# Optimization experiments

Measured on AMD Instinct MI355X. Metric: run time of the kernel, lower is better.

The kernel has to match this reference:

```python
import jax, jax.numpy as jnp
import numpy as np

B, L, C = 32, 4096, 64
PL, PC = 64, 16          # patch sizes along L and C
NP = 256                 # num_patches
OUT = 512                # output_dim
FS = 1000.0              # sampling frequency -> T = 1/FS


def setup_inputs() -> dict:
    key = jax.random.key(0)
    ks = jax.random.split(key, 7)
    d_in = PL * (PC * 2)
    return {
        "x": jax.random.normal(ks[0], (B, L, C), dtype=jnp.float32),
        "start_L": jax.random.randint(ks[1], (B, NP), 0, L - PL + 1, dtype=jnp.int32),
        "start_C": jax.random.randint(ks[2], (B, NP), 0, C - PC + 1, dtype=jnp.int32),
        "w1": jax.random.normal(ks[3], (OUT, d_in), dtype=jnp.float32) / np.sqrt(d_in),
        "b1": jax.random.normal(ks[4], (OUT,), dtype=jnp.float32) * 0.01,
        "w2": jax.random.normal(ks[5], (OUT, OUT), dtype=jnp.float32) / np.sqrt(OUT),
        "b2": jax.random.normal(ks[6], (OUT,), dtype=jnp.float32) * 0.01,
    }


def reference(x, start_L, start_C, w1, b1, w2, b2):
    T = 1.0 / FS
    t = jnp.arange(L, dtype=jnp.float32) * T                      # [L]

    # patch index grids (wrapping, as in the torch module)
    idx_L = (start_L[:, :, None] + jnp.arange(PL, dtype=jnp.int32)) % L   # [B,NP,PL]
    idx_C = (start_C[:, :, None] + jnp.arange(PC, dtype=jnp.int32)) % C   # [B,NP,PC]

    # double gather: patches[b,p,i,j] = x[b, idx_L[b,p,i], idx_C[b,p,j]]
    b_idx = jnp.arange(B, dtype=jnp.int32)[:, None, None, None]
    patches = x[b_idx, idx_L[:, :, :, None], idx_C[:, :, None, :]]        # [B,NP,PL,PC]

    # time embedding gathered with the same L indices, broadcast over PC
    t_patches = jnp.broadcast_to(t[idx_L][:, :, :, None], (B, NP, PL, PC))

    feats = jnp.concatenate([patches, t_patches], axis=-1)                # [B,NP,PL,2*PC]
    feats = feats.reshape(B, NP, PL * 2 * PC)

    h = jnp.einsum('bpd,od->bpo', feats, w1) + b1
    h = jax.nn.silu(h)
    out = jnp.einsum('bpo,qo->bpq', h, w2) + b2                           # [B,NP,OUT]
    return out
```

## Files before the change

kernel.cpp:

```cpp
#include <hip/hip_runtime.h>
#include <hip/hip_bf16.h>
#include <stdint.h>

#define BB   32
#define LL   4096
#define CCH  64
#define PLh  64
#define PCh  16
#define NPp  256
#define DOUT 512
#define DINX 1024
#define MM   (BB * NPp)
#define TT   0.001f

using bf16 = __hip_bfloat16;
typedef __attribute__((ext_vector_type(8))) short bf16x8;
typedef __attribute__((ext_vector_type(4))) float f32x4;

__device__ __forceinline__ void async_copy16(void* lds, const void* g) {
    __builtin_amdgcn_global_load_lds(
        (const __attribute__((address_space(1))) void*)g,
        (__attribute__((address_space(3))) void*)lds,
        16, 0, 0);
}

__global__ __launch_bounds__(256) void convert_f32_bf16(
    const float* __restrict__ in, bf16* __restrict__ out, int n)
{
    int i = (blockIdx.x * 256 + threadIdx.x) * 4;
    if (i >= n) return;
    float4 v = *(const float4*)(in + i);
    union { bf16 h[4]; uint2 u; } p;
    p.h[0] = __float2bfloat16(v.x);
    p.h[1] = __float2bfloat16(v.y);
    p.h[2] = __float2bfloat16(v.z);
    p.h[3] = __float2bfloat16(v.w);
    *(uint2*)(out + i) = p.u;
}

__global__ __launch_bounds__(256) void convert_w1x(
    const float* __restrict__ w1, bf16* __restrict__ w1x)
{
    int i = (blockIdx.x * 256 + threadIdx.x) * 4;
    int o = i >> 10, r = i & 1023;
    int l = r >> 4, j = r & 15;
    float4 v = *(const float4*)(w1 + (size_t)o * 2048 + l * 32 + j);
    union { bf16 h[4]; uint2 u; } p;
    p.h[0] = __float2bfloat16(v.x);
    p.h[1] = __float2bfloat16(v.y);
    p.h[2] = __float2bfloat16(v.z);
    p.h[3] = __float2bfloat16(v.w);
    *(uint2*)(w1x + i) = p.u;
}

__global__ __launch_bounds__(64) void precompute_affine(
    const float* __restrict__ w1, const float* __restrict__ b1,
    float* __restrict__ A1, float* __restrict__ C1)
{
    const int o = blockIdx.x;
    const int l = threadIdx.x;
    const float* wr = w1 + (size_t)o * 2048 + l * 32 + 16;
    float s0 = 0.f;
#pragma unroll
    for (int j = 0; j < 16; ++j) s0 += wr[j];
    float s1 = (float)l * s0;
#pragma unroll
    for (int off = 32; off > 0; off >>= 1) {
        s0 += __shfl_down(s0, off);
        s1 += __shfl_down(s1, off);
    }
    if (l == 0) {
        A1[o] = TT * s0;
        C1[o] = b1[o] + TT * s1;
    }
}

__global__ __launch_bounds__(256) void gather_feats(
    const float* __restrict__ x, const int* __restrict__ startL,
    const int* __restrict__ startC, bf16* __restrict__ feats)
{
    const int m = blockIdx.x;
    const int b = m >> 8;
    const int t = threadIdx.x;
    const int l = t >> 2;
    const int j0 = (t & 3) * 4;
    const int sl = startL[m];
    const int sc = startC[m];
    const float* src = x + ((size_t)b * LL + (size_t)(sl + l)) * CCH + sc + j0;
    union { bf16 h[4]; uint2 u; } p;
#pragma unroll
    for (int i = 0; i < 4; ++i) p.h[i] = __float2bfloat16(src[i]);
    *(uint2*)(feats + (size_t)m * DINX + t * 4) = p.u;
}

template <bool FUSE1>
__global__ __launch_bounds__(256) void gemm_bt(
    const bf16* __restrict__ A,
    const bf16* __restrict__ Bt,
    const float* __restrict__ bias,
    const float* __restrict__ C1,
    const int*   __restrict__ sL,
    void* __restrict__ outp,
    const int N, const int K)
{
    constexpr int BK = 32;
    __shared__ __align__(16) bf16 As[64 * BK];
    __shared__ __align__(16) bf16 Bs[64 * BK];

    const int tid  = threadIdx.x;
    const int lane = tid & 63;
    const int wave = tid >> 6;
    const int row0 = blockIdx.x * 64;
    const int col0 = blockIdx.y * 64;

    const int  srow  = wave * 16 + (lane >> 2);
    const int  skoff = (lane & 3) * 8;
    const bf16* agp = A  + (size_t)(row0 + srow) * K + skoff;
    const bf16* bgp = Bt + (size_t)(col0 + srow) * K + skoff;
    bf16* as_dst = &As[wave * 16 * BK];
    bf16* bs_dst = &Bs[wave * 16 * BK];

    const int mw = (wave >> 1) * 32;
    const int nw = (wave & 1) * 32;
    const int fr = lane & 15;
    const int fq = lane >> 4;

    f32x4 acc[2][2] = {};

    for (int k0 = 0; k0 < K; k0 += BK) {
        __syncthreads();
        async_copy16(as_dst, agp + k0);
        async_copy16(bs_dst, bgp + k0);
        __syncthreads();

        bf16x8 af[2], bfm[2];
#pragma unroll
        for (int i = 0; i < 2; ++i)
            af[i] = *(const bf16x8*)&As[(mw + i * 16 + fr) * BK + fq * 8];
#pragma unroll
        for (int j = 0; j < 2; ++j)
            bfm[j] = *(const bf16x8*)&Bs[(nw + j * 16 + fr) * BK + fq * 8];
#pragma unroll
        for (int i = 0; i < 2; ++i)
#pragma unroll
            for (int j = 0; j < 2; ++j)
                acc[i][j] = __builtin_amdgcn_mfma_f32_16x16x32_bf16(
                    af[i], bfm[j], acc[i][j], 0, 0, 0);
    }

    float slr[2][4];
    if (FUSE1) {
#pragma unroll
        for (int i = 0; i < 2; ++i)
#pragma unroll
            for (int r = 0; r < 4; ++r)
                slr[i][r] = (float)sL[row0 + mw + i * 16 + fq * 4 + r];
    }

#pragma unroll
    for (int j = 0; j < 2; ++j) {
        const int col = col0 + nw + j * 16 + fr;
        const float bv = bias[col];
        const float cv = FUSE1 ? C1[col] : 0.f;
#pragma unroll
        for (int i = 0; i < 2; ++i) {
#pragma unroll
            for (int r = 0; r < 4; ++r) {
                const int row = row0 + mw + i * 16 + fq * 4 + r;
                float v;
                if (FUSE1) {
                    v = acc[i][j][r] + slr[i][r] * bv + cv;
                    v = v / (1.0f + __expf(-v));
                    ((bf16*)outp)[(size_t)row * N + col] = __float2bfloat16(v);
                } else {
                    v = acc[i][j][r] + bv;
                    ((float*)outp)[(size_t)row * N + col] = v;
                }
            }
        }
    }
}

extern "C" void kernel_launch(void* const* d_in, const int* in_sizes, int n_in,
                              void* d_out, int out_size, void* d_ws, size_t ws_size,
                              hipStream_t stream)
{
    const float* x  = (const float*)d_in[0];
    const int*   sL = (const int*)  d_in[1];
    const int*   sC = (const int*)  d_in[2];
    const float* w1 = (const float*)d_in[3];
    const float* b1 = (const float*)d_in[4];
    const float* w2 = (const float*)d_in[5];
    const float* b2 = (const float*)d_in[6];
    float* out = (float*)d_out;

    char* ws = (char*)d_ws;
    bf16* featsB = (bf16*)ws;
    size_t off = (size_t)MM * DINX * 2;
    bf16* w1xB = (bf16*)(ws + off); off += (size_t)DOUT * DINX * 2;
    bf16* w2B  = (bf16*)(ws + off); off += (size_t)DOUT * DOUT * 2;
    bf16* hB   = (bf16*)(ws + off); off += (size_t)MM * DOUT * 2;
    float* A1  = (float*)(ws + off); off += DOUT * 4;
    float* C1  = (float*)(ws + off);

    convert_w1x<<<(DOUT * DINX / 4 + 255) / 256, 256, 0, stream>>>(w1, w1xB);
    convert_f32_bf16<<<(DOUT * DOUT / 4 + 255) / 256, 256, 0, stream>>>(w2, w2B, DOUT * DOUT);
    precompute_affine<<<DOUT, 64, 0, stream>>>(w1, b1, A1, C1);
    gather_feats<<<MM, 256, 0, stream>>>(x, sL, sC, featsB);

    gemm_bt<true><<<dim3(MM / 64, DOUT / 64), 256, 0, stream>>>(
        featsB, w1xB, A1, C1, sL, hB, DOUT, DINX);

    gemm_bt<false><<<dim3(MM / 64, DOUT / 64), 256, 0, stream>>>(
        hB, w2B, b2, nullptr, nullptr, out, DOUT, DOUT);
}
```

Before: 133.7 us.

## Double-buffer GEMM with BK=64, merge prep kernels, vectorize gather

The GEMM kernel now uses BK=64 with two LDS buffers, issuing the async global-to-LDS loads for the next K tile while the current tile's MFMAs run, and drops one barrier per iteration. The three weight-preparation kernels are merged into a single launch. The gather kernel now has one thread per patch row doing four float4 loads and two 16-byte stores. These changes aim to cut the load-latency stalls, barrier count and launch overhead in exchange for more LDS per block; relying on the single barrier to order async LDS writes against reads of the other buffer is a potential hazard.

```diff
diff --git a/kernel.cpp b/kernel.cpp
--- a/kernel.cpp
+++ b/kernel.cpp
@@ -5,8 +5,6 @@
 #define BB   32
 #define LL   4096
 #define CCH  64
-#define PLh  64
-#define PCh  16
 #define NPp  256
 #define DOUT 512
 #define DINX 1024
@@ -24,54 +22,49 @@
         16, 0, 0);
 }
 
-__global__ __launch_bounds__(256) void convert_f32_bf16(
-    const float* __restrict__ in, bf16* __restrict__ out, int n)
-{
-    int i = (blockIdx.x * 256 + threadIdx.x) * 4;
-    if (i >= n) return;
-    float4 v = *(const float4*)(in + i);
+__device__ __forceinline__ uint2 pack4_bf16(float a, float b, float c, float d) {
     union { bf16 h[4]; uint2 u; } p;
-    p.h[0] = __float2bfloat16(v.x);
-    p.h[1] = __float2bfloat16(v.y);
-    p.h[2] = __float2bfloat16(v.z);
-    p.h[3] = __float2bfloat16(v.w);
-    *(uint2*)(out + i) = p.u;
-}
-
-__global__ __launch_bounds__(256) void convert_w1x(
-    const float* __restrict__ w1, bf16* __restrict__ w1x)
-{
-    int i = (blockIdx.x * 256 + threadIdx.x) * 4;
-    int o = i >> 10, r = i & 1023;
-    int l = r >> 4, j = r & 15;
-    float4 v = *(const float4*)(w1 + (size_t)o * 2048 + l * 32 + j);
-    union { bf16 h[4]; uint2 u; } p;
-    p.h[0] = __float2bfloat16(v.x);
-    p.h[1] = __float2bfloat16(v.y);
-    p.h[2] = __float2bfloat16(v.z);
-    p.h[3] = __float2bfloat16(v.w);
-    *(uint2*)(w1x + i) = p.u;
-}
-
-__global__ __launch_bounds__(64) void precompute_affine(
+    p.h[0] = __float2bfloat16(a);
+    p.h[1] = __float2bfloat16(b);
+    p.h[2] = __float2bfloat16(c);
+    p.h[3] = __float2bfloat16(d);
+    return p.u;
+}
+
+__global__ __launch_bounds__(256) void prep(
     const float* __restrict__ w1, const float* __restrict__ b1,
+    const float* __restrict__ w2,
+    bf16* __restrict__ w1x, bf16* __restrict__ w2b,
     float* __restrict__ A1, float* __restrict__ C1)
 {
-    const int o = blockIdx.x;
-    const int l = threadIdx.x;
-    const float* wr = w1 + (size_t)o * 2048 + l * 32 + 16;
-    float s0 = 0.f;
-#pragma unroll
-    for (int j = 0; j < 16; ++j) s0 += wr[j];
-    float s1 = (float)l * s0;
-#pragma unroll
-    for (int off = 32; off > 0; off >>= 1) {
-        s0 += __shfl_down(s0, off);
-        s1 += __shfl_down(s1, off);
-    }
-    if (l == 0) {
-        A1[o] = TT * s0;
-        C1[o] = b1[o] + TT * s1;
+    const int blk = blockIdx.x;
+    if (blk < 512) {
+        int i = (blk * 256 + threadIdx.x) * 4;
+        int o = i >> 10, r = i & 1023;
+        int l = r >> 4, j = r & 15;
+        float4 v = *(const float4*)(w1 + (size_t)o * 2048 + l * 32 + j);
+        *(uint2*)(w1x + i) = pack4_bf16(v.x, v.y, v.z, v.w);
+    } else if (blk < 768) {
+        int i = ((blk - 512) * 256 + threadIdx.x) * 4;
+        float4 v = *(const float4*)(w2 + i);
+        *(uint2*)(w2b + i) = pack4_bf16(v.x, v.y, v.z, v.w);
+    } else {
+        const int o = (blk - 768) * 4 + (threadIdx.x >> 6);
+        const int l = threadIdx.x & 63;
+        const float* wr = w1 + (size_t)o * 2048 + l * 32 + 16;
+        float s0 = 0.f;
+#pragma unroll
+        for (int j = 0; j < 16; ++j) s0 += wr[j];
+        float s1 = (float)l * s0;
+#pragma unroll
+        for (int off = 32; off > 0; off >>= 1) {
+            s0 += __shfl_down(s0, off);
+            s1 += __shfl_down(s1, off);
+        }
+        if (l == 0) {
+            A1[o] = TT * s0;
+            C1[o] = b1[o] + TT * s1;
+        }
     }
 }
 
@@ -79,33 +72,41 @@
     const float* __restrict__ x, const int* __restrict__ startL,
     const int* __restrict__ startC, bf16* __restrict__ feats)
 {
-    const int m = blockIdx.x;
+    const int m = blockIdx.x * 4 + (threadIdx.x >> 6);
     const int b = m >> 8;
-    const int t = threadIdx.x;
-    const int l = t >> 2;
-    const int j0 = (t & 3) * 4;
+    const int l = threadIdx.x & 63;
     const int sl = startL[m];
     const int sc = startC[m];
-    const float* src = x + ((size_t)b * LL + (size_t)(sl + l)) * CCH + sc + j0;
-    union { bf16 h[4]; uint2 u; } p;
-#pragma unroll
-    for (int i = 0; i < 4; ++i) p.h[i] = __float2bfloat16(src[i]);
-    *(uint2*)(feats + (size_t)m * DINX + t * 4) = p.u;
+    const float* src = x + ((size_t)b * LL + (size_t)(sl + l)) * CCH + sc;
+    float4 v0 = *(const float4*)(src);
+    float4 v1 = *(const float4*)(src + 4);
+    float4 v2 = *(const float4*)(src + 8);
+    float4 v3 = *(const float4*)(src + 12);
+    uint4 p0, p1;
+    uint2 a = pack4_bf16(v0.x, v0.y, v0.z, v0.w);
+    uint2 c = pack4_bf16(v1.x, v1.y, v1.z, v1.w);
+    p0.x = a.x; p0.y = a.y; p0.z = c.x; p0.w = c.y;
+    a = pack4_bf16(v2.x, v2.y, v2.z, v2.w);
+    c = pack4_bf16(v3.x, v3.y, v3.z, v3.w);
+    p1.x = a.x; p1.y = a.y; p1.z = c.x; p1.w = c.y;
+    bf16* dst = feats + (size_t)m * DINX + l * 16;
+    *(uint4*)dst       = p0;
+    *(uint4*)(dst + 8) = p1;
 }
 
 template <bool FUSE1>
-__global__ __launch_bounds__(256) void gemm_bt(
+__global__ __launch_bounds__(256, 4) void gemm_db(
     const bf16* __restrict__ A,
     const bf16* __restrict__ Bt,
-    const float* __restrict__ bias,
+    const float* __restrict__ P1,
     const float* __restrict__ C1,
     const int*   __restrict__ sL,
     void* __restrict__ outp,
     const int N, const int K)
 {
-    constexpr int BK = 32;
-    __shared__ __align__(16) bf16 As[64 * BK];
-    __shared__ __align__(16) bf16 Bs[64 * BK];
+    constexpr int BK = 64;
+    __shared__ __align__(16) bf16 As[2][64 * BK];
+    __shared__ __align__(16) bf16 Bs[2][64 * BK];
 
     const int tid  = threadIdx.x;
     const int lane = tid & 63;
@@ -113,12 +114,11 @@
     const int row0 = blockIdx.x * 64;
     const int col0 = blockIdx.y * 64;
 
-    const int  srow  = wave * 16 + (lane >> 2);
-    const int  skoff = (lane & 3) * 8;
+    const int  srow  = wave * 16 + (lane >> 3);
+    const int  skoff = (lane & 7) * 8;
     const bf16* agp = A  + (size_t)(row0 + srow) * K + skoff;
     const bf16* bgp = Bt + (size_t)(col0 + srow) * K + skoff;
-    bf16* as_dst = &As[wave * 16 * BK];
-    bf16* bs_dst = &Bs[wave * 16 * BK];
+    const int w16 = wave * 16;
 
     const int mw = (wave >> 1) * 32;
     const int nw = (wave & 1) * 32;
@@ -127,25 +127,44 @@
 
     f32x4 acc[2][2] = {};
 
-    for (int k0 = 0; k0 < K; k0 += BK) {
+    const int nIter = K / BK;
+
+    async_copy16(&As[0][(w16 + 0) * BK], agp);
+    async_copy16(&As[0][(w16 + 8) * BK], agp + (size_t)8 * K);
+    async_copy16(&Bs[0][(w16 + 0) * BK], bgp);
+    async_copy16(&Bs[0][(w16 + 8) * BK], bgp + (size_t)8 * K);
+
+    for (int it = 0; it < nIter; ++it) {
         __syncthreads();
-        async_copy16(as_dst, agp + k0);
-        async_copy16(bs_dst, bgp + k0);
-        __syncthreads();
-
-        bf16x8 af[2], bfm[2];
+        const int cur = it & 1;
+        if (it + 1 < nIter) {
+            const int nxt = cur ^ 1;
+            const int k1 = (it + 1) * BK;
+            async_copy16(&As[nxt][(w16 + 0) * BK], agp + k1);
+            async_copy16(&As[nxt][(w16 + 8) * BK], agp + (size_t)8 * K + k1);
+            async_copy16(&Bs[nxt][(w16 + 0) * BK], bgp + k1);
+            async_copy16(&Bs[nxt][(w16 + 8) * BK], bgp + (size_t)8 * K + k1);
+        }
+
+        bf16x8 af[2][2], bfr[2][2];
 #pragma unroll
         for (int i = 0; i < 2; ++i)
-            af[i] = *(const bf16x8*)&As[(mw + i * 16 + fr) * BK + fq * 8];
+#pragma unroll
+            for (int ks = 0; ks < 2; ++ks)
+                af[i][ks] = *(const bf16x8*)&As[cur][(mw + i * 16 + fr) * BK + ks * 32 + fq * 8];
 #pragma unroll
         for (int j = 0; j < 2; ++j)
-            bfm[j] = *(const bf16x8*)&Bs[(nw + j * 16 + fr) * BK + fq * 8];
-#pragma unroll
-        for (int i = 0; i < 2; ++i)
-#pragma unroll
-            for (int j = 0; j < 2; ++j)
-                acc[i][j] = __builtin_amdgcn_mfma_f32_16x16x32_bf16(
-                    af[i], bfm[j], acc[i][j], 0, 0, 0);
+#pragma unroll
+            for (int ks = 0; ks < 2; ++ks)
+                bfr[j][ks] = *(const bf16x8*)&Bs[cur][(nw + j * 16 + fr) * BK + ks * 32 + fq * 8];
+#pragma unroll
+        for (int ks = 0; ks < 2; ++ks)
+#pragma unroll
+            for (int i = 0; i < 2; ++i)
+#pragma unroll
+                for (int j = 0; j < 2; ++j)
+                    acc[i][j] = __builtin_amdgcn_mfma_f32_16x16x32_bf16(
+                        af[i][ks], bfr[j][ks], acc[i][j], 0, 0, 0);
     }
 
     float slr[2][4];
@@ -156,28 +175,24 @@
             for (int r = 0; r < 4; ++r)
                 slr[i][r] = (float)sL[row0 + mw + i * 16 + fq * 4 + r];
     }
-
 #pragma unroll
     for (int j = 0; j < 2; ++j) {
         const int col = col0 + nw + j * 16 + fr;
-        const float bv = bias[col];
+        const float bv = P1[col];
         const float cv = FUSE1 ? C1[col] : 0.f;
 #pragma unroll
-        for (int i = 0; i < 2; ++i) {
+        for (int i = 0; i < 2; ++i)
 #pragma unroll
             for (int r = 0; r < 4; ++r) {
                 const int row = row0 + mw + i * 16 + fq * 4 + r;
-                float v;
                 if (FUSE1) {
-                    v = acc[i][j][r] + slr[i][r] * bv + cv;
+                    float v = acc[i][j][r] + slr[i][r] * bv + cv;
                     v = v / (1.0f + __expf(-v));
                     ((bf16*)outp)[(size_t)row * N + col] = __float2bfloat16(v);
                 } else {
-                    v = acc[i][j][r] + bv;
-                    ((float*)outp)[(size_t)row * N + col] = v;
+                    ((float*)outp)[(size_t)row * N + col] = acc[i][j][r] + bv;
                 }
             }
-        }
     }
 }
 
@@ -195,22 +210,19 @@
     float* out = (float*)d_out;
 
     char* ws = (char*)d_ws;
-    bf16* featsB = (bf16*)ws;
-    size_t off = (size_t)MM * DINX * 2;
-    bf16* w1xB = (bf16*)(ws + off); off += (size_t)DOUT * DINX * 2;
-    bf16* w2B  = (bf16*)(ws + off); off += (size_t)DOUT * DOUT * 2;
-    bf16* hB   = (bf16*)(ws + off); off += (size_t)MM * DOUT * 2;
-    float* A1  = (float*)(ws + off); off += DOUT * 4;
-    float* C1  = (float*)(ws + off);
-
-    convert_w1x<<<(DOUT * DINX / 4 + 255) / 256, 256, 0, stream>>>(w1, w1xB);
-    convert_f32_bf16<<<(DOUT * DOUT / 4 + 255) / 256, 256, 0, stream>>>(w2, w2B, DOUT * DOUT);
-    precompute_affine<<<DOUT, 64, 0, stream>>>(w1, b1, A1, C1);
-    gather_feats<<<MM, 256, 0, stream>>>(x, sL, sC, featsB);
-
-    gemm_bt<true><<<dim3(MM / 64, DOUT / 64), 256, 0, stream>>>(
-        featsB, w1xB, A1, C1, sL, hB, DOUT, DINX);
-
-    gemm_bt<false><<<dim3(MM / 64, DOUT / 64), 256, 0, stream>>>(
-        hB, w2B, b2, nullptr, nullptr, out, DOUT, DOUT);
-}
+    bf16* featsB = (bf16*)ws;                      size_t off = (size_t)MM * DINX * 2;
+    bf16* w1x = (bf16*)(ws + off);                 off += (size_t)DOUT * DINX * 2;
+    bf16* w2b = (bf16*)(ws + off);                 off += (size_t)DOUT * DOUT * 2;
+    bf16* hB  = (bf16*)(ws + off);                 off += (size_t)MM * DOUT * 2;
+    float* A1 = (float*)(ws + off);                off += DOUT * 4;
+    float* C1 = (float*)(ws + off);
+
+    prep<<<896, 256, 0, stream>>>(w1, b1, w2, w1x, w2b, A1, C1);
+    gather_feats<<<MM / 4, 256, 0, stream>>>(x, sL, sC, featsB);
+
+    gemm_db<true><<<dim3(MM / 64, DOUT / 64), 256, 0, stream>>>(
+        featsB, w1x, A1, C1, sL, hB, DOUT, DINX);
+
+    gemm_db<false><<<dim3(MM / 64, DOUT / 64), 256, 0, stream>>>(
+        hB, w2b, b2, nullptr, nullptr, out, DOUT, DOUT);
+}
```

Result: no change. 134.2 us (+0.4%).
